# Kernel tuning notes

Measured on AMD Instinct MI355X. Metric: run time of the kernel, lower is better.

The kernel has to match this reference:

```python
import jax, jax.numpy as jnp
import numpy as np

B, S, E, H = 2, 2048, 1024, 16
HD = E // H            # head_dim = 64
ROT = 64               # rotary_dim == head_dim
BASE = 10000.0


def setup_inputs() -> dict:
    key = jax.random.key(0)
    k1, k2, k3, k4, k5 = jax.random.split(key, 5)
    return {
        "x": jax.random.normal(k1, (B, S, E), dtype=jnp.float32),
        "mask": jnp.ones((B, S), dtype=jnp.int32),
        "qkv_w": jax.random.normal(k2, (3 * E, E), dtype=jnp.float32) * (1.0 / np.sqrt(E)),
        "qkv_b": jax.random.normal(k3, (3 * E,), dtype=jnp.float32) * 0.02,
        "out_w": jax.random.normal(k4, (E, E), dtype=jnp.float32) * (1.0 / np.sqrt(E)),
        "out_b": jax.random.normal(k5, (E,), dtype=jnp.float32) * 0.02,
    }


def _rotate_half(x):
    # split last dim into (even, odd) pairs and rotate 90 degrees
    x = x.reshape(*x.shape[:-1], -1, 2)
    x1, x2 = x[..., 0], x[..., 1]
    return jnp.stack((-x2, x1), axis=-1).reshape(*x.shape[:-2], -1)


def _rope_cos_sin(seq_len, rot_dim, dtype):
    inv_freq = 1.0 / (BASE ** (jnp.arange(0, rot_dim, 2, dtype=jnp.float32) / rot_dim))
    freqs = jnp.arange(seq_len, dtype=jnp.float32)[:, None] * inv_freq[None, :]  # [S, rot/2]
    cos = jnp.repeat(jnp.cos(freqs), 2, axis=-1).astype(dtype)  # [S, rot]
    sin = jnp.repeat(jnp.sin(freqs), 2, axis=-1).astype(dtype)
    return cos, sin


def reference(x, mask, qkv_w, qkv_b, out_w, out_b):
    b, s, _ = x.shape
    qkv = x @ qkv_w.T + qkv_b                      # [B,S,3E]
    q, k, v = jnp.split(qkv, 3, axis=-1)
    shape = lambda t: t.reshape(b, s, H, HD).transpose(0, 2, 1, 3)  # [B,H,S,HD]
    q, k, v = shape(q), shape(k), shape(v)

    cos, sin = _rope_cos_sin(s, ROT, q.dtype)      # [S, ROT]
    cos = cos[None, None]                          # [1,1,S,ROT]
    sin = sin[None, None]
    q_rot, q_pass = q[..., :ROT], q[..., ROT:]
    k_rot, k_pass = k[..., :ROT], k[..., ROT:]
    q = jnp.concatenate((q_rot * cos + _rotate_half(q_rot) * sin, q_pass), axis=-1)
    k = jnp.concatenate((k_rot * cos + _rotate_half(k_rot) * sin, k_pass), axis=-1)

    scale = 1.0 / np.sqrt(HD)
    scores = jnp.einsum("bhqd,bhkd->bhqk", q, k) * scale  # [B,H,S,S]
    keep = (mask != 0)[:, None, None, :]           # [B,1,1,S]
    scores = jnp.where(keep, scores, -jnp.inf)
    attn = jax.nn.softmax(scores, axis=-1)
    context = jnp.einsum("bhqk,bhkd->bhqd", attn, v)
    context = context.transpose(0, 2, 1, 3).reshape(b, s, E)
    return context @ out_w.T + out_b
```

## Files before the change

kernel.cpp:

```cpp
#include <hip/hip_runtime.h>
#include <hip/hip_bf16.h>
#include <cmath>

#define SB 2048
#define EB 1024
#define NH 16
#define HD 64
#define KLOG 0.14391156831212788f

typedef unsigned short u16;
typedef unsigned int u32;
typedef __attribute__((ext_vector_type(8))) short short8;
typedef __attribute__((ext_vector_type(4))) float f32x4;

__device__ __forceinline__ u16 f2b(float x) {
  __hip_bfloat16 h = __float2bfloat16(x);
  return *reinterpret_cast<u16*>(&h);
}

__device__ __forceinline__ void gl_lds16(const u16* g, u16* l) {
  __builtin_amdgcn_global_load_lds(
      (const __attribute__((address_space(1))) unsigned int*)g,
      (__attribute__((address_space(3))) unsigned int*)l, 16, 0, 0);
}

#define CN1 (4096 * 1024 / 4)
#define CN2 (3072 * 1024 / 4)
#define CN3 (1024 * 1024 / 4)
__global__ __launch_bounds__(256) void conv_all(
    const float* __restrict__ x, const float* __restrict__ w1,
    const float* __restrict__ w2, u16* __restrict__ xb,
    u16* __restrict__ wqb, u16* __restrict__ owb) {
  int i = blockIdx.x * 256 + threadIdx.x;
  const float* src;
  u16* dst;
  int j;
  if (i < CN1) { src = x; dst = xb; j = i; }
  else if (i < CN1 + CN2) { src = w1; dst = wqb; j = i - CN1; }
  else if (i < CN1 + CN2 + CN3) { src = w2; dst = owb; j = i - CN1 - CN2; }
  else return;
  float4 v = ((const float4*)src)[j];
  ushort4 o;
  o.x = f2b(v.x); o.y = f2b(v.y); o.z = f2b(v.z); o.w = f2b(v.w);
  ((ushort4*)dst)[j] = o;
}

__global__ __launch_bounds__(256) void qkv_mfma_rope(
    const u16* __restrict__ A, const u16* __restrict__ Bw,
    const float* __restrict__ bias, u16* __restrict__ qb,
    u16* __restrict__ kb, u16* __restrict__ vt) {
  __shared__ u16 As[128 * 32];
  __shared__ u16 Bs[128 * 32];
  __shared__ float CS[128 * 32];
  __shared__ float SN[128 * 32];

  const int t = threadIdx.x;
  const int lane = t & 63, wv = t >> 6;
  const int l15 = lane & 15, quad = lane >> 4;
  const int wm = wv >> 1, wn = wv & 1;
  const int m0 = blockIdx.x * 128;
  const int n0 = blockIdx.y * 128;

  f32x4 acc[4][4] = {};

  for (int k0 = 0; k0 < 1024; k0 += 32) {
#pragma unroll
    for (int c = 0; c < 2; c++) {
      int r = wv * 32 + c * 16;
      const u16* ga = A + (size_t)(m0 + r + (lane >> 2)) * 1024 + k0 + (lane & 3) * 8;
      const u16* gb = Bw + (size_t)(n0 + r + (lane >> 2)) * 1024 + k0 + (lane & 3) * 8;
      gl_lds16(ga, &As[r * 32]);
      gl_lds16(gb, &Bs[r * 32]);
    }
    __syncthreads();

    short8 a[4], b[4];
#pragma unroll
    for (int mi = 0; mi < 4; mi++)
      a[mi] = *(const short8*)&As[(wm * 64 + mi * 16 + l15) * 32 + quad * 8];
#pragma unroll
    for (int ni = 0; ni < 4; ni++)
      b[ni] = *(const short8*)&Bs[(wn * 64 + ni * 16 + l15) * 32 + quad * 8];
#pragma unroll
    for (int mi = 0; mi < 4; mi++)
#pragma unroll
      for (int ni = 0; ni < 4; ni++)
        acc[mi][ni] = __builtin_amdgcn_mfma_f32_16x16x32_bf16(a[mi], b[ni], acc[mi][ni], 0, 0, 0);
    __syncthreads();
  }

  const int n_base = n0 + wn * 64;
  const int which = n_base >> 10;
  float b4[4];
#pragma unroll
  for (int ni = 0; ni < 4; ni++) b4[ni] = bias[n_base + ni * 16 + l15];

  if (which < 2) {
#pragma unroll
    for (int i = 0; i < 16; i++) {
      int idx = t + i * 256;
      int row = idx >> 5, p = idx & 31;
      float spos = (float)((m0 & 2047) + row);
      float theta = spos * expf(-(float)(2 * p) * KLOG);
      float sn_, cs_;
      sincosf(theta, &sn_, &cs_);
      CS[idx] = cs_; SN[idx] = sn_;
    }
    __syncthreads();
  }

  const int h = (n_base & 1023) >> 6;
#pragma unroll
  for (int mi = 0; mi < 4; mi++) {
#pragma unroll
    for (int r = 0; r < 4; r++) {
      int row = wm * 64 + mi * 16 + quad * 4 + r;
      int m = m0 + row;
      int bb = m >> 11, s = m & 2047;
      if (which < 2) {
        u16* dst = (which == 0) ? qb : kb;
        size_t obase = ((size_t)(bb * NH + h) * SB + s) * HD;
#pragma unroll
        for (int ni = 0; ni < 4; ni++) {
          float v = acc[mi][ni][r] + b4[ni];
          int d = ni * 16 + l15;
          float pv = __shfl_xor(v, 1, 64);
          float c = CS[row * 32 + (d >> 1)];
          float sn_ = SN[row * 32 + (d >> 1)];
          v = v * c + pv * ((d & 1) ? sn_ : -sn_);
          if (which == 0) v *= 0.125f;
          dst[obase + d] = f2b(v);
        }
      } else {
        size_t tbase = (size_t)(bb * NH + h) * HD;
#pragma unroll
        for (int ni = 0; ni < 4; ni++) {
          float v = acc[mi][ni][r] + b4[ni];
          int d = ni * 16 + l15;
          vt[(tbase + d) * SB + s] = f2b(v);
        }
      }
    }
  }
}

__global__ __launch_bounds__(512, 4) void attn_mfma(
    const u16* __restrict__ qb, const u16* __restrict__ kb,
    const u16* __restrict__ vt, const int* __restrict__ mask,
    u16* __restrict__ ctx) {
  __shared__ u16 Ks[2][64][72];
  __shared__ u16 Vt[2][64][72];
  __shared__ u32 Ps2[8][32][20];
  __shared__ int mks[2][64];

  const int bh = blockIdx.x, b = bh >> 4, h = bh & 15;
  const int q0 = blockIdx.y * 128;
  const int t = threadIdx.x;
  const int lane = t & 63, wv = t >> 6;
  const int l15 = lane & 15, quad = lane >> 4;

  short8 bq[2];
  {
    const u16* qp = qb + ((size_t)bh * SB + q0 + wv * 16 + l15) * HD;
    bq[0] = *(const short8*)&qp[quad * 8];
    bq[1] = *(const short8*)&qp[32 + quad * 8];
  }

  const u16* kbase = kb + (size_t)bh * SB * HD;
  const u16* vbase = vt + (size_t)bh * HD * SB;
  const int* mbase = mask + b * SB;

  const int sr = t >> 3, sc = t & 7;

  uint4 kreg = *(const uint4*)&kbase[(size_t)sr * HD + sc * 8];
  uint4 vreg = *(const uint4*)&vbase[(size_t)sr * SB + sc * 8];
  int mreg = (t < 64) ? mbase[t] : 0;

  f32x4 o[4] = {};
  float m_i = -INFINITY, l_i = 0.f;

  for (int kt = 0; kt < SB / 64; kt++) {
    const int bufi = kt & 1;
    *(uint4*)&Ks[bufi][sr][sc * 8] = kreg;
    *(uint4*)&Vt[bufi][sr][sc * 8] = vreg;
    if (t < 64) mks[bufi][t] = mreg;
    __syncthreads();

    if (kt + 1 < SB / 64) {
      kreg = *(const uint4*)&kbase[(size_t)((kt + 1) * 64 + sr) * HD + sc * 8];
      vreg = *(const uint4*)&vbase[(size_t)sr * SB + (kt + 1) * 64 + sc * 8];
      if (t < 64) mreg = mbase[(kt + 1) * 64 + t];
    }

    f32x4 s[4] = {};
#pragma unroll
    for (int mb = 0; mb < 4; mb++) {
      short8 a0 = *(const short8*)&Ks[bufi][mb * 16 + l15][quad * 8];
      short8 a1 = *(const short8*)&Ks[bufi][mb * 16 + l15][32 + quad * 8];
      s[mb] = __builtin_amdgcn_mfma_f32_16x16x32_bf16(a0, bq[0], s[mb], 0, 0, 0);
      s[mb] = __builtin_amdgcn_mfma_f32_16x16x32_bf16(a1, bq[1], s[mb], 0, 0, 0);
    }

    float mx = -INFINITY;
#pragma unroll
    for (int mb = 0; mb < 4; mb++) {
      int4 mv = *(const int4*)&mks[bufi][mb * 16 + quad * 4];
      int mk4[4] = {mv.x, mv.y, mv.z, mv.w};
#pragma unroll
      for (int r = 0; r < 4; r++) {
        float sv = mk4[r] ? s[mb][r] : -INFINITY;
        s[mb][r] = sv;
        mx = fmaxf(mx, sv);
      }
    }
    mx = fmaxf(mx, __shfl_xor(mx, 16, 64));
    mx = fmaxf(mx, __shfl_xor(mx, 32, 64));
    float mn = fmaxf(m_i, mx);
    float mn_s = (mn == -INFINITY) ? 0.f : mn;
    float a = __expf(m_i - mn_s);
    float rs = 0.f;
#pragma unroll
    for (int mb = 0; mb < 4; mb++)
#pragma unroll
      for (int r = 0; r < 4; r++) {
        float p = __expf(s[mb][r] - mn_s);
        s[mb][r] = p;
        rs += p;
      }
    rs += __shfl_xor(rs, 16, 64);
    rs += __shfl_xor(rs, 32, 64);
    l_i = l_i * a + rs;
    m_i = mn;

#pragma unroll
    for (int mb = 0; mb < 4; mb++)
#pragma unroll
      for (int pr = 0; pr < 2; pr++) {
        u32 pk = (u32)f2b(s[mb][2 * pr]) | ((u32)f2b(s[mb][2 * pr + 1]) << 16);
        Ps2[wv][mb * 8 + quad * 2 + pr][l15] = pk;
      }
    short8 pb[2];
#pragma unroll
    for (int kk = 0; kk < 2; kk++) {
      u32 w[4];
#pragma unroll
      for (int j = 0; j < 4; j++)
        w[j] = Ps2[wv][kk * 16 + quad * 4 + j][l15];
      pb[kk] = *(const short8*)w;
    }

#pragma unroll
    for (int nb = 0; nb < 4; nb++) {
      short8 v0 = *(const short8*)&Vt[bufi][nb * 16 + l15][quad * 8];
      short8 v1 = *(const short8*)&Vt[bufi][nb * 16 + l15][32 + quad * 8];
#pragma unroll
      for (int r = 0; r < 4; r++) o[nb][r] *= a;
      o[nb] = __builtin_amdgcn_mfma_f32_16x16x32_bf16(v0, pb[0], o[nb], 0, 0, 0);
      o[nb] = __builtin_amdgcn_mfma_f32_16x16x32_bf16(v1, pb[1], o[nb], 0, 0, 0);
    }
  }

  {
    float linv = 1.f / l_i;
    int qrow = q0 + wv * 16 + l15;
    size_t base = ((size_t)b * SB + qrow) * EB + h * HD;
#pragma unroll
    for (int nb = 0; nb < 4; nb++)
#pragma unroll
      for (int pr = 0; pr < 2; pr++) {
        int d = nb * 16 + quad * 4 + 2 * pr;
        u32 pk = (u32)f2b(o[nb][2 * pr] * linv) |
                 ((u32)f2b(o[nb][2 * pr + 1] * linv) << 16);
        *(u32*)&ctx[base + d] = pk;
      }
  }
}

__global__ __launch_bounds__(256) void out_mfma(
    const u16* __restrict__ A, const u16* __restrict__ Bw,
    const float* __restrict__ bias, float* __restrict__ out) {
  __shared__ u16 As[128 * 32];
  __shared__ u16 Bs[128 * 32];

  const int t = threadIdx.x;
  const int lane = t & 63, wv = t >> 6;
  const int l15 = lane & 15, quad = lane >> 4;
  const int wm = wv >> 1, wn = wv & 1;
  const int m0 = blockIdx.x * 128;
  const int n0 = blockIdx.y * 128;

  f32x4 acc[4][4] = {};

  for (int k0 = 0; k0 < 1024; k0 += 32) {
#pragma unroll
    for (int c = 0; c < 2; c++) {
      int r = wv * 32 + c * 16;
      const u16* ga = A + (size_t)(m0 + r + (lane >> 2)) * 1024 + k0 + (lane & 3) * 8;
      const u16* gb = Bw + (size_t)(n0 + r + (lane >> 2)) * 1024 + k0 + (lane & 3) * 8;
      gl_lds16(ga, &As[r * 32]);
      gl_lds16(gb, &Bs[r * 32]);
    }
    __syncthreads();

    short8 a[4], b[4];
#pragma unroll
    for (int mi = 0; mi < 4; mi++)
      a[mi] = *(const short8*)&As[(wm * 64 + mi * 16 + l15) * 32 + quad * 8];
#pragma unroll
    for (int ni = 0; ni < 4; ni++)
      b[ni] = *(const short8*)&Bs[(wn * 64 + ni * 16 + l15) * 32 + quad * 8];
#pragma unroll
    for (int mi = 0; mi < 4; mi++)
#pragma unroll
      for (int ni = 0; ni < 4; ni++)
        acc[mi][ni] = __builtin_amdgcn_mfma_f32_16x16x32_bf16(a[mi], b[ni], acc[mi][ni], 0, 0, 0);
    __syncthreads();
  }

  float b4[4];
#pragma unroll
  for (int ni = 0; ni < 4; ni++) b4[ni] = bias[n0 + wn * 64 + ni * 16 + l15];
#pragma unroll
  for (int mi = 0; mi < 4; mi++)
#pragma unroll
    for (int r = 0; r < 4; r++) {
      int m = m0 + wm * 64 + mi * 16 + quad * 4 + r;
#pragma unroll
      for (int ni = 0; ni < 4; ni++)
        out[(size_t)m * 1024 + n0 + wn * 64 + ni * 16 + l15] = acc[mi][ni][r] + b4[ni];
    }
}

extern "C" void kernel_launch(void* const* d_in, const int* in_sizes, int n_in,
                              void* d_out, int out_size, void* d_ws, size_t ws_size,
                              hipStream_t stream) {
  const float* x     = (const float*)d_in[0];
  const int* mask    = (const int*)d_in[1];
  const float* qkv_w = (const float*)d_in[2];
  const float* qkv_b = (const float*)d_in[3];
  const float* out_w = (const float*)d_in[4];
  const float* out_b = (const float*)d_in[5];
  float* out = (float*)d_out;

  char* wsb = (char*)d_ws;
  u16* xb  = (u16*)wsb;
  u16* wqb = (u16*)(wsb + ( 8ull << 20));
  u16* owb = (u16*)(wsb + (14ull << 20));
  u16* qb  = (u16*)(wsb + (16ull << 20));
  u16* kb  = (u16*)(wsb + (24ull << 20));
  u16* vtb = (u16*)(wsb + (32ull << 20));
  u16* cxb = (u16*)(wsb + (40ull << 20));

  dim3 blk(256);
  hipLaunchKernelGGL(conv_all, dim3((CN1 + CN2 + CN3 + 255) / 256), blk, 0, stream,
                     x, qkv_w, out_w, xb, wqb, owb);

  hipLaunchKernelGGL(qkv_mfma_rope, dim3(32, 24), blk, 0, stream,
                     xb, wqb, qkv_b, qb, kb, vtb);

  hipLaunchKernelGGL(attn_mfma, dim3(32, 16), dim3(512), 0, stream,
                     qb, kb, vtb, mask, cxb);

  hipLaunchKernelGGL(out_mfma, dim3(32, 8), blk, 0, stream, cxb, owb, out_b, out);
}
```

Before: 213.6 us.

## Precompute RoPE tables, widen attention key tiles, use exp2 softmax, shrink output tiles

RoPE cos/sin tables are now computed once in the conversion kernel and loaded into the QKV GEMM epilogue, replacing per-block sincos work. V-transpose stores are packed into 4-wide writes. The attention kernel processes 128 keys per iteration with single-buffered LDS, an additive mask bias, and exp2f with log2e folded into the Q scale. The output GEMM uses 64-row tiles to launch twice as many blocks. These cut transcendental work and loop overhead and raise occupancy, at the cost of more registers and less load/compute overlap in attention.

```diff
diff --git a/kernel.cpp b/kernel.cpp
--- a/kernel.cpp
+++ b/kernel.cpp
@@ -7,6 +7,7 @@
 #define NH 16
 #define HD 64
 #define KLOG 0.14391156831212788f
+#define QSC 0.18033688011112042f
 
 typedef unsigned short u16;
 typedef unsigned int u32;
@@ -27,27 +28,40 @@
 #define CN1 (4096 * 1024 / 4)
 #define CN2 (3072 * 1024 / 4)
 #define CN3 (1024 * 1024 / 4)
+#define CNS (CN1 + CN2 + CN3)
 __global__ __launch_bounds__(256) void conv_all(
     const float* __restrict__ x, const float* __restrict__ w1,
     const float* __restrict__ w2, u16* __restrict__ xb,
-    u16* __restrict__ wqb, u16* __restrict__ owb) {
+    u16* __restrict__ wqb, u16* __restrict__ owb,
+    float* __restrict__ ctab, float* __restrict__ stab) {
   int i = blockIdx.x * 256 + threadIdx.x;
-  const float* src;
-  u16* dst;
-  int j;
-  if (i < CN1) { src = x; dst = xb; j = i; }
-  else if (i < CN1 + CN2) { src = w1; dst = wqb; j = i - CN1; }
-  else if (i < CN1 + CN2 + CN3) { src = w2; dst = owb; j = i - CN1 - CN2; }
-  else return;
-  float4 v = ((const float4*)src)[j];
-  ushort4 o;
-  o.x = f2b(v.x); o.y = f2b(v.y); o.z = f2b(v.z); o.w = f2b(v.w);
-  ((ushort4*)dst)[j] = o;
+  if (i < CNS) {
+    const float* src;
+    u16* dst;
+    int j;
+    if (i < CN1) { src = x; dst = xb; j = i; }
+    else if (i < CN1 + CN2) { src = w1; dst = wqb; j = i - CN1; }
+    else { src = w2; dst = owb; j = i - CN1 - CN2; }
+    float4 v = ((const float4*)src)[j];
+    ushort4 o;
+    o.x = f2b(v.x); o.y = f2b(v.y); o.z = f2b(v.z); o.w = f2b(v.w);
+    ((ushort4*)dst)[j] = o;
+  } else {
+    int j = i - CNS;
+    if (j < SB * 32) {
+      int pos = j >> 5, p = j & 31;
+      float th = (float)pos * expf(-(float)(2 * p) * KLOG);
+      float sn, cs;
+      sincosf(th, &sn, &cs);
+      ctab[j] = cs; stab[j] = sn;
+    }
+  }
 }
 
 __global__ __launch_bounds__(256) void qkv_mfma_rope(
     const u16* __restrict__ A, const u16* __restrict__ Bw,
-    const float* __restrict__ bias, u16* __restrict__ qb,
+    const float* __restrict__ bias, const float* __restrict__ ctab,
+    const float* __restrict__ stab, u16* __restrict__ qb,
     u16* __restrict__ kb, u16* __restrict__ vt) {
   __shared__ u16 As[128 * 32];
   __shared__ u16 Bs[128 * 32];
@@ -95,30 +109,27 @@
 #pragma unroll
   for (int ni = 0; ni < 4; ni++) b4[ni] = bias[n_base + ni * 16 + l15];
 
+  {
+    int base = (m0 & 2047) * 32;
+#pragma unroll
+    for (int i = 0; i < 4; i++) {
+      int idx = (t + i * 256) * 4;
+      *(float4*)&CS[idx] = *(const float4*)&ctab[base + idx];
+      *(float4*)&SN[idx] = *(const float4*)&stab[base + idx];
+    }
+  }
+  __syncthreads();
+
+  const int h = (n_base & 1023) >> 6;
+  const int bb = m0 >> 11;
   if (which < 2) {
-#pragma unroll
-    for (int i = 0; i < 16; i++) {
-      int idx = t + i * 256;
-      int row = idx >> 5, p = idx & 31;
-      float spos = (float)((m0 & 2047) + row);
-      float theta = spos * expf(-(float)(2 * p) * KLOG);
-      float sn_, cs_;
-      sincosf(theta, &sn_, &cs_);
-      CS[idx] = cs_; SN[idx] = sn_;
-    }
-    __syncthreads();
-  }
-
-  const int h = (n_base & 1023) >> 6;
-#pragma unroll
-  for (int mi = 0; mi < 4; mi++) {
-#pragma unroll
-    for (int r = 0; r < 4; r++) {
-      int row = wm * 64 + mi * 16 + quad * 4 + r;
-      int m = m0 + row;
-      int bb = m >> 11, s = m & 2047;
-      if (which < 2) {
-        u16* dst = (which == 0) ? qb : kb;
+    u16* dst = (which == 0) ? qb : kb;
+#pragma unroll
+    for (int mi = 0; mi < 4; mi++) {
+#pragma unroll
+      for (int r = 0; r < 4; r++) {
+        int row = wm * 64 + mi * 16 + quad * 4 + r;
+        int s = (m0 & 2047) + row;
         size_t obase = ((size_t)(bb * NH + h) * SB + s) * HD;
 #pragma unroll
         for (int ni = 0; ni < 4; ni++) {
@@ -128,17 +139,25 @@
           float c = CS[row * 32 + (d >> 1)];
           float sn_ = SN[row * 32 + (d >> 1)];
           v = v * c + pv * ((d & 1) ? sn_ : -sn_);
-          if (which == 0) v *= 0.125f;
+          if (which == 0) v *= QSC;
           dst[obase + d] = f2b(v);
         }
-      } else {
-        size_t tbase = (size_t)(bb * NH + h) * HD;
-#pragma unroll
-        for (int ni = 0; ni < 4; ni++) {
-          float v = acc[mi][ni][r] + b4[ni];
-          int d = ni * 16 + l15;
-          vt[(tbase + d) * SB + s] = f2b(v);
-        }
+      }
+    }
+  } else {
+    size_t tbase = (size_t)(bb * NH + h) * HD;
+#pragma unroll
+    for (int mi = 0; mi < 4; mi++) {
+      int s0 = (m0 & 2047) + wm * 64 + mi * 16 + quad * 4;
+#pragma unroll
+      for (int ni = 0; ni < 4; ni++) {
+        int d = ni * 16 + l15;
+        ushort4 pk;
+        pk.x = f2b(acc[mi][ni][0] + b4[ni]);
+        pk.y = f2b(acc[mi][ni][1] + b4[ni]);
+        pk.z = f2b(acc[mi][ni][2] + b4[ni]);
+        pk.w = f2b(acc[mi][ni][3] + b4[ni]);
+        *(ushort4*)&vt[(tbase + d) * SB + s0] = pk;
       }
     }
   }
@@ -148,10 +167,10 @@
     const u16* __restrict__ qb, const u16* __restrict__ kb,
     const u16* __restrict__ vt, const int* __restrict__ mask,
     u16* __restrict__ ctx) {
-  __shared__ u16 Ks[2][64][72];
-  __shared__ u16 Vt[2][64][72];
+  __shared__ u16 Ks[128][72];
+  __shared__ u16 Vt[64][136];
   __shared__ u32 Ps2[8][32][20];
-  __shared__ int mks[2][64];
+  __shared__ float fb[128];
 
   const int bh = blockIdx.x, b = bh >> 4, h = bh & 15;
   const int q0 = blockIdx.y * 128;
@@ -170,45 +189,46 @@
   const u16* vbase = vt + (size_t)bh * HD * SB;
   const int* mbase = mask + b * SB;
 
-  const int sr = t >> 3, sc = t & 7;
-
-  uint4 kreg = *(const uint4*)&kbase[(size_t)sr * HD + sc * 8];
-  uint4 vreg = *(const uint4*)&vbase[(size_t)sr * SB + sc * 8];
-  int mreg = (t < 64) ? mbase[t] : 0;
+  const int kr0 = t >> 3, kc0 = t & 7;
+  const int kr1 = 64 + (t >> 3);
+  const int vd0 = t >> 4, vc0 = t & 15;
+  const int vd1 = 32 + (t >> 4);
+
+  uint4 kreg0 = *(const uint4*)&kbase[(size_t)kr0 * HD + kc0 * 8];
+  uint4 kreg1 = *(const uint4*)&kbase[(size_t)kr1 * HD + kc0 * 8];
+  uint4 vreg0 = *(const uint4*)&vbase[(size_t)vd0 * SB + vc0 * 8];
+  uint4 vreg1 = *(const uint4*)&vbase[(size_t)vd1 * SB + vc0 * 8];
+  float freg = (t < 128) ? (mbase[t] ? 0.f : -1e9f) : 0.f;
 
   f32x4 o[4] = {};
-  float m_i = -INFINITY, l_i = 0.f;
-
-  for (int kt = 0; kt < SB / 64; kt++) {
-    const int bufi = kt & 1;
-    *(uint4*)&Ks[bufi][sr][sc * 8] = kreg;
-    *(uint4*)&Vt[bufi][sr][sc * 8] = vreg;
-    if (t < 64) mks[bufi][t] = mreg;
-    __syncthreads();
-
-    if (kt + 1 < SB / 64) {
-      kreg = *(const uint4*)&kbase[(size_t)((kt + 1) * 64 + sr) * HD + sc * 8];
-      vreg = *(const uint4*)&vbase[(size_t)sr * SB + (kt + 1) * 64 + sc * 8];
-      if (t < 64) mreg = mbase[(kt + 1) * 64 + t];
-    }
-
-    f32x4 s[4] = {};
-#pragma unroll
-    for (int mb = 0; mb < 4; mb++) {
-      short8 a0 = *(const short8*)&Ks[bufi][mb * 16 + l15][quad * 8];
-      short8 a1 = *(const short8*)&Ks[bufi][mb * 16 + l15][32 + quad * 8];
-      s[mb] = __builtin_amdgcn_mfma_f32_16x16x32_bf16(a0, bq[0], s[mb], 0, 0, 0);
-      s[mb] = __builtin_amdgcn_mfma_f32_16x16x32_bf16(a1, bq[1], s[mb], 0, 0, 0);
-    }
-
-    float mx = -INFINITY;
-#pragma unroll
-    for (int mb = 0; mb < 4; mb++) {
-      int4 mv = *(const int4*)&mks[bufi][mb * 16 + quad * 4];
-      int mk4[4] = {mv.x, mv.y, mv.z, mv.w};
+  float m_i = -1e30f, l_i = 0.f;
+
+  for (int kt = 0; kt < SB / 128; kt++) {
+    __syncthreads();
+    *(uint4*)&Ks[kr0][kc0 * 8] = kreg0;
+    *(uint4*)&Ks[kr1][kc0 * 8] = kreg1;
+    *(uint4*)&Vt[vd0][vc0 * 8] = vreg0;
+    *(uint4*)&Vt[vd1][vc0 * 8] = vreg1;
+    if (t < 128) fb[t] = freg;
+    __syncthreads();
+
+    f32x4 s[8];
+#pragma unroll
+    for (int mb = 0; mb < 8; mb++) {
+      short8 a0 = *(const short8*)&Ks[mb * 16 + l15][quad * 8];
+      short8 a1 = *(const short8*)&Ks[mb * 16 + l15][32 + quad * 8];
+      f32x4 z = {};
+      z = __builtin_amdgcn_mfma_f32_16x16x32_bf16(a0, bq[0], z, 0, 0, 0);
+      s[mb] = __builtin_amdgcn_mfma_f32_16x16x32_bf16(a1, bq[1], z, 0, 0, 0);
+    }
+
+    float mx = -1e30f;
+#pragma unroll
+    for (int mb = 0; mb < 8; mb++) {
+      f32x4 bias4 = *(const f32x4*)&fb[mb * 16 + quad * 4];
 #pragma unroll
       for (int r = 0; r < 4; r++) {
-        float sv = mk4[r] ? s[mb][r] : -INFINITY;
+        float sv = s[mb][r] + bias4[r];
         s[mb][r] = sv;
         mx = fmaxf(mx, sv);
       }
@@ -216,14 +236,13 @@
     mx = fmaxf(mx, __shfl_xor(mx, 16, 64));
     mx = fmaxf(mx, __shfl_xor(mx, 32, 64));
     float mn = fmaxf(m_i, mx);
-    float mn_s = (mn == -INFINITY) ? 0.f : mn;
-    float a = __expf(m_i - mn_s);
+    float a = exp2f(m_i - mn);
     float rs = 0.f;
 #pragma unroll
-    for (int mb = 0; mb < 4; mb++)
+    for (int mb = 0; mb < 8; mb++)
 #pragma unroll
       for (int r = 0; r < 4; r++) {
-        float p = __expf(s[mb][r] - mn_s);
+        float p = exp2f(s[mb][r] - mn);
         s[mb][r] = p;
         rs += p;
       }
@@ -232,31 +251,46 @@
     l_i = l_i * a + rs;
     m_i = mn;
 
-#pragma unroll
-    for (int mb = 0; mb < 4; mb++)
-#pragma unroll
-      for (int pr = 0; pr < 2; pr++) {
-        u32 pk = (u32)f2b(s[mb][2 * pr]) | ((u32)f2b(s[mb][2 * pr + 1]) << 16);
-        Ps2[wv][mb * 8 + quad * 2 + pr][l15] = pk;
-      }
-    short8 pb[2];
-#pragma unroll
-    for (int kk = 0; kk < 2; kk++) {
-      u32 w[4];
-#pragma unroll
-      for (int j = 0; j < 4; j++)
-        w[j] = Ps2[wv][kk * 16 + quad * 4 + j][l15];
-      pb[kk] = *(const short8*)w;
-    }
-
-#pragma unroll
-    for (int nb = 0; nb < 4; nb++) {
-      short8 v0 = *(const short8*)&Vt[bufi][nb * 16 + l15][quad * 8];
-      short8 v1 = *(const short8*)&Vt[bufi][nb * 16 + l15][32 + quad * 8];
+    if (kt + 1 < SB / 128) {
+      size_t ko = (size_t)(kt + 1) * 128;
+      kreg0 = *(const uint4*)&kbase[(ko + kr0) * HD + kc0 * 8];
+      kreg1 = *(const uint4*)&kbase[(ko + kr1) * HD + kc0 * 8];
+      vreg0 = *(const uint4*)&vbase[(size_t)vd0 * SB + ko + vc0 * 8];
+      vreg1 = *(const uint4*)&vbase[(size_t)vd1 * SB + ko + vc0 * 8];
+      if (t < 128) freg = mbase[ko + t] ? 0.f : -1e9f;
+    }
+
+#pragma unroll
+    for (int nb = 0; nb < 4; nb++)
 #pragma unroll
       for (int r = 0; r < 4; r++) o[nb][r] *= a;
-      o[nb] = __builtin_amdgcn_mfma_f32_16x16x32_bf16(v0, pb[0], o[nb], 0, 0, 0);
-      o[nb] = __builtin_amdgcn_mfma_f32_16x16x32_bf16(v1, pb[1], o[nb], 0, 0, 0);
+
+#pragma unroll
+    for (int hh = 0; hh < 2; hh++) {
+#pragma unroll
+      for (int mb2 = 0; mb2 < 4; mb2++)
+#pragma unroll
+        for (int pr = 0; pr < 2; pr++) {
+          int mb = hh * 4 + mb2;
+          u32 pk = (u32)f2b(s[mb][2 * pr]) | ((u32)f2b(s[mb][2 * pr + 1]) << 16);
+          Ps2[wv][mb2 * 8 + quad * 2 + pr][l15] = pk;
+        }
+      short8 pb[2];
+#pragma unroll
+      for (int kk = 0; kk < 2; kk++) {
+        u32 w[4];
+#pragma unroll
+        for (int j = 0; j < 4; j++)
+          w[j] = Ps2[wv][kk * 16 + quad * 4 + j][l15];
+        pb[kk] = *(const short8*)w;
+      }
+#pragma unroll
+      for (int nb = 0; nb < 4; nb++) {
+        short8 v0 = *(const short8*)&Vt[nb * 16 + l15][hh * 64 + quad * 8];
+        short8 v1 = *(const short8*)&Vt[nb * 16 + l15][hh * 64 + 32 + quad * 8];
+        o[nb] = __builtin_amdgcn_mfma_f32_16x16x32_bf16(v0, pb[0], o[nb], 0, 0, 0);
+        o[nb] = __builtin_amdgcn_mfma_f32_16x16x32_bf16(v1, pb[1], o[nb], 0, 0, 0);
+      }
     }
   }
 
@@ -279,38 +313,40 @@
 __global__ __launch_bounds__(256) void out_mfma(
     const u16* __restrict__ A, const u16* __restrict__ Bw,
     const float* __restrict__ bias, float* __restrict__ out) {
-  __shared__ u16 As[128 * 32];
+  __shared__ u16 As[64 * 32];
   __shared__ u16 Bs[128 * 32];
 
   const int t = threadIdx.x;
   const int lane = t & 63, wv = t >> 6;
   const int l15 = lane & 15, quad = lane >> 4;
   const int wm = wv >> 1, wn = wv & 1;
-  const int m0 = blockIdx.x * 128;
+  const int m0 = blockIdx.x * 64;
   const int n0 = blockIdx.y * 128;
 
-  f32x4 acc[4][4] = {};
+  f32x4 acc[2][4] = {};
 
   for (int k0 = 0; k0 < 1024; k0 += 32) {
-#pragma unroll
-    for (int c = 0; c < 2; c++) {
-      int r = wv * 32 + c * 16;
-      const u16* ga = A + (size_t)(m0 + r + (lane >> 2)) * 1024 + k0 + (lane & 3) * 8;
-      const u16* gb = Bw + (size_t)(n0 + r + (lane >> 2)) * 1024 + k0 + (lane & 3) * 8;
-      gl_lds16(ga, &As[r * 32]);
-      gl_lds16(gb, &Bs[r * 32]);
-    }
-    __syncthreads();
-
-    short8 a[4], b[4];
-#pragma unroll
-    for (int mi = 0; mi < 4; mi++)
-      a[mi] = *(const short8*)&As[(wm * 64 + mi * 16 + l15) * 32 + quad * 8];
+    {
+      const u16* ga = A + (size_t)(m0 + wv * 16 + (lane >> 2)) * 1024 + k0 + (lane & 3) * 8;
+      gl_lds16(ga, &As[(wv * 16) * 32]);
+#pragma unroll
+      for (int c = 0; c < 2; c++) {
+        int r = wv * 32 + c * 16;
+        const u16* gb = Bw + (size_t)(n0 + r + (lane >> 2)) * 1024 + k0 + (lane & 3) * 8;
+        gl_lds16(gb, &Bs[r * 32]);
+      }
+    }
+    __syncthreads();
+
+    short8 a[2], b[4];
+#pragma unroll
+    for (int mi = 0; mi < 2; mi++)
+      a[mi] = *(const short8*)&As[(wm * 32 + mi * 16 + l15) * 32 + quad * 8];
 #pragma unroll
     for (int ni = 0; ni < 4; ni++)
       b[ni] = *(const short8*)&Bs[(wn * 64 + ni * 16 + l15) * 32 + quad * 8];
 #pragma unroll
-    for (int mi = 0; mi < 4; mi++)
+    for (int mi = 0; mi < 2; mi++)
 #pragma unroll
       for (int ni = 0; ni < 4; ni++)
         acc[mi][ni] = __builtin_amdgcn_mfma_f32_16x16x32_bf16(a[mi], b[ni], acc[mi][ni], 0, 0, 0);
@@ -321,10 +357,10 @@
 #pragma unroll
   for (int ni = 0; ni < 4; ni++) b4[ni] = bias[n0 + wn * 64 + ni * 16 + l15];
 #pragma unroll
-  for (int mi = 0; mi < 4; mi++)
+  for (int mi = 0; mi < 2; mi++)
 #pragma unroll
     for (int r = 0; r < 4; r++) {
-      int m = m0 + wm * 64 + mi * 16 + quad * 4 + r;
+      int m = m0 + wm * 32 + mi * 16 + quad * 4 + r;
 #pragma unroll
       for (int ni = 0; ni < 4; ni++)
         out[(size_t)m * 1024 + n0 + wn * 64 + ni * 16 + l15] = acc[mi][ni][r] + b4[ni];
@@ -343,23 +379,26 @@
   float* out = (float*)d_out;
 
   char* wsb = (char*)d_ws;
-  u16* xb  = (u16*)wsb;
-  u16* wqb = (u16*)(wsb + ( 8ull << 20));
-  u16* owb = (u16*)(wsb + (14ull << 20));
-  u16* qb  = (u16*)(wsb + (16ull << 20));
-  u16* kb  = (u16*)(wsb + (24ull << 20));
-  u16* vtb = (u16*)(wsb + (32ull << 20));
-  u16* cxb = (u16*)(wsb + (40ull << 20));
+  u16* xb    = (u16*)wsb;
+  u16* wqb   = (u16*)(wsb + ( 8ull << 20));
+  u16* owb   = (u16*)(wsb + (14ull << 20));
+  u16* qb    = (u16*)(wsb + (16ull << 20));
+  u16* kb    = (u16*)(wsb + (24ull << 20));
+  u16* vtb   = (u16*)(wsb + (32ull << 20));
+  u16* cxb   = (u16*)(wsb + (40ull << 20));
+  float* ctab = (float*)(wsb + (48ull << 20));
+  float* stab = (float*)(wsb + (48ull << 20) + (256u << 10));
 
   dim3 blk(256);
-  hipLaunchKernelGGL(conv_all, dim3((CN1 + CN2 + CN3 + 255) / 256), blk, 0, stream,
-                     x, qkv_w, out_w, xb, wqb, owb);
+  int convBlocks = (CNS + SB * 32 + 255) / 256;
+  hipLaunchKernelGGL(conv_all, dim3(convBlocks), blk, 0, stream,
+                     x, qkv_w, out_w, xb, wqb, owb, ctab, stab);
 
   hipLaunchKernelGGL(qkv_mfma_rope, dim3(32, 24), blk, 0, stream,
-                     xb, wqb, qkv_b, qb, kb, vtb);
+                     xb, wqb, qkv_b, ctab, stab, qb, kb, vtb);
 
   hipLaunchKernelGGL(attn_mfma, dim3(32, 16), dim3(512), 0, stream,
                      qb, kb, vtb, mask, cxb);
 
-  hipLaunchKernelGGL(out_mfma, dim3(32, 8), blk, 0, stream, cxb, owb, out_b, out);
-}
+  hipLaunchKernelGGL(out_mfma, dim3(64, 8), blk, 0, stream, cxb, owb, out_b, out);
+}
```

New measurement: 236.2 us. 10.6% more time.
